# Kernel tuning notes

Hardware: AMD Instinct MI355X
Metric: run time of the kernel (lower is better)

The kernel has to match this reference:

```python
import jax, jax.numpy as jnp
import numpy as np

DIM = 1024
N_HEADS = 16
HEAD_DIM = DIM // N_HEADS
B, S = 1, 4096


def setup_inputs() -> dict:
    key = jax.random.key(0)
    kx, kq, kk, kv, ko = jax.random.split(key, 5)
    scale = 1.0 / np.sqrt(DIM)
    return {
        "x": jax.random.normal(kx, (B, S, DIM), dtype=jnp.float32),
        "Wq": jax.random.normal(kq, (DIM, DIM), dtype=jnp.float32) * scale,
        "Wk": jax.random.normal(kk, (DIM, DIM), dtype=jnp.float32) * scale,
        "Wv": jax.random.normal(kv, (DIM, DIM), dtype=jnp.float32) * scale,
        "Wo": jax.random.normal(ko, (DIM, DIM), dtype=jnp.float32) * scale,
    }


def reference(x, Wq, Wk, Wv, Wo):
    Bb, Ss, D = x.shape
    H, hd = N_HEADS, HEAD_DIM
    # nn.Linear(dim, dim, bias=False): y = x @ W.T
    q = (x @ Wq.T).reshape(Bb, Ss, H, hd).transpose(0, 2, 1, 3)  # [B,H,S,hd]
    k = (x @ Wk.T).reshape(Bb, Ss, H, hd).transpose(0, 2, 1, 3)
    v = (x @ Wv.T).reshape(Bb, Ss, H, hd).transpose(0, 2, 1, 3)
    scores = jnp.einsum("bhqd,bhkd->bhqk", q, k) / np.sqrt(hd)  # [B,H,S,S]
    causal = jnp.triu(jnp.ones((Ss, Ss), dtype=bool), 1)
    scores = jnp.where(causal, -jnp.inf, scores)
    # max-subtract softmax (stable); jax.nn.softmax does the same subtraction
    attn = jax.nn.softmax(scores, axis=-1)
    z = jnp.einsum("bhqk,bhkd->bhqd", attn, v)  # [B,H,S,hd]
    z = z.transpose(0, 2, 1, 3).reshape(Bb, Ss, D)
    return z @ Wo.T
```

## Files before the change

### kernel.cpp

```cpp
#include <hip/hip_runtime.h>
#include <hip/hip_bf16.h>

#define DIM   1024
#define NHEAD 16
#define HD    64
#define SEQ   4096

typedef __attribute__((ext_vector_type(4))) float  f32x4;
typedef __attribute__((ext_vector_type(8))) __bf16 bf16x8;
typedef __attribute__((ext_vector_type(8))) _Float16 f16x8;
typedef __attribute__((ext_vector_type(4))) short  short4v;
typedef __attribute__((ext_vector_type(4))) unsigned uint4v;

template <int B> struct ICt { static constexpr int v = B; };

static __device__ __forceinline__ short f2bf(float f) {
  unsigned u = __builtin_bit_cast(unsigned, f);
  u += 0x7fffu + ((u >> 16) & 1u);
  return (short)(u >> 16);
}
static __device__ __forceinline__ float bflo(unsigned u) {
  return __builtin_bit_cast(float, u << 16);
}
static __device__ __forceinline__ float bfhi(unsigned u) {
  return __builtin_bit_cast(float, u & 0xFFFF0000u);
}

static __device__ __forceinline__ unsigned pkf16(float a, float b) {
  return __builtin_bit_cast(unsigned, __builtin_amdgcn_cvt_pkrtz(a, b));
}

static __device__ __forceinline__ void gl2lds16(const void* g, void* l) {
  __builtin_amdgcn_global_load_lds(
      (__attribute__((address_space(1))) void*)g,
      (__attribute__((address_space(3))) void*)l, 16, 0, 0);
}

__global__ void cast_kernel(const float* __restrict__ x,
                            const float* __restrict__ Wq,
                            const float* __restrict__ Wk,
                            const float* __restrict__ Wv,
                            const float* __restrict__ Wo,
                            short* __restrict__ xb,
                            short* __restrict__ wb) {
  int b = blockIdx.x;
  const float* src;
  short* dst;
  if (b < 4096) {
    src = x + (size_t)b * 1024;
    dst = xb + (size_t)b * 1024;
  } else {
    int t = b - 4096;
    int w = t >> 10;
    size_t off = (size_t)(t & 1023) * 1024;
    src = (w == 0 ? Wq : w == 1 ? Wk : w == 2 ? Wv : Wo) + off;
    dst = wb + (size_t)w * 1048576 + off;
  }
  int i = threadIdx.x;
  float4 v = ((const float4*)src)[i];
  short4v o;
  o.x = f2bf(v.x); o.y = f2bf(v.y); o.z = f2bf(v.z); o.w = f2bf(v.w);
  ((short4v*)dst)[i] = o;
}

template <int OUT>
static __device__ __forceinline__ void gemm_tile(const short* __restrict__ A,
                                                 const short* __restrict__ B,
                                                 void* __restrict__ Cv,
                                                 int N, int K, int bm, int bn,
                                                 short* As, short* Bs) {
  const int tid  = threadIdx.x;
  const int wave = tid >> 6;
  const int lane = tid & 63;
  const int quad = lane >> 4;
  const int l15  = lane & 15;
  const int wm = (wave >> 1) * 64;
  const int wn = (wave & 1) * 64;
  const int sw = (quad ^ ((l15 >> 1) & 3)) * 8;

  f32x4 acc[4][4];
#pragma unroll
  for (int i = 0; i < 4; ++i)
#pragma unroll
    for (int j = 0; j < 4; ++j) acc[i][j] = (f32x4){0.f, 0.f, 0.f, 0.f};

  for (int k0 = 0; k0 < K; k0 += 32) {
#pragma unroll
    for (int it = 0; it < 2; ++it) {
      int c   = it * 256 + wave * 64 + lane;
      int row = c >> 2;
      int ce  = ((c & 3) ^ ((c >> 3) & 3)) * 8;
      gl2lds16(A + (size_t)(bm + row) * K + k0 + ce,
               As + (size_t)(it * 256 + wave * 64) * 8);
      gl2lds16(B + (size_t)(bn + row) * K + k0 + ce,
               Bs + (size_t)(it * 256 + wave * 64) * 8);
    }
    __syncthreads();

    bf16x8 af[4], bfr[4];
#pragma unroll
    for (int mt = 0; mt < 4; ++mt)
      af[mt] = *(const bf16x8*)&As[(wm + mt * 16 + l15) * 32 + sw];
#pragma unroll
    for (int nt = 0; nt < 4; ++nt)
      bfr[nt] = *(const bf16x8*)&Bs[(wn + nt * 16 + l15) * 32 + sw];
#pragma unroll
    for (int mt = 0; mt < 4; ++mt)
#pragma unroll
      for (int nt = 0; nt < 4; ++nt)
        acc[mt][nt] = __builtin_amdgcn_mfma_f32_16x16x32_bf16(
            af[mt], bfr[nt], acc[mt][nt], 0, 0, 0);
    __syncthreads();
  }

  short* C = (short*)Cv;
#pragma unroll
  for (int mt = 0; mt < 4; ++mt)
#pragma unroll
    for (int nt = 0; nt < 4; ++nt)
#pragma unroll
      for (int r = 0; r < 4; ++r) {
        size_t idx = (size_t)(bm + wm + mt * 16 + quad * 4 + r) * N +
                     bn + wn + nt * 16 + l15;
        if (OUT == 0)
          C[idx] = f2bf(acc[mt][nt][r]);
        else
          C[idx] = (short)(pkf16(acc[mt][nt][r], 0.f) & 0xFFFFu);
      }
}

__global__ __launch_bounds__(256, 2) void proj_kernel(const short* __restrict__ xb,
                                                      const short* __restrict__ wqk,
                                                      const short* __restrict__ wv,
                                                      short* __restrict__ QKb,
                                                      short* __restrict__ Vtb) {
  __shared__ short As[128 * 32];
  __shared__ short Bs[128 * 32];
  int b = blockIdx.x;
  if (b < 512) {
    gemm_tile<0>(xb, wqk, QKb, 2048, 1024, (b >> 4) * 128, (b & 15) * 128, As, Bs);
  } else {
    int t = b - 512;
    gemm_tile<2>(wv, xb, Vtb, 4096, 1024, (t >> 5) * 128, (t & 31) * 128, As, Bs);
  }
}

__global__ __launch_bounds__(512, 4) void flash_attn(const short* __restrict__ QK,
                                                     const short* __restrict__ Vt,
                                                     short* __restrict__ pO0,
                                                     short* __restrict__ pO1,
                                                     short* __restrict__ pO2,
                                                     short* __restrict__ pO3,
                                                     float* __restrict__ lp) {
  const int bb  = blockIdx.x;
  const int z   = bb & 3;
  const int h   = (bb >> 2) & 15;
  const int y   = 15 - (bb >> 6);

  __shared__ short Ks[2 * 4096];
  __shared__ short Vs[2 * 4096];

  const int wave = threadIdx.x >> 6;
  const int lane = threadIdx.x & 63;
  const int quad = lane >> 4;
  const int l15  = lane & 15;
  const int qw   = y * 256 + wave * 32;
  const int jtd  = 4 * y + (wave >> 1);

  const short* Qp = QK + h * HD;
  const short* Kp = QK + 1024 + h * HD;
  const short* Vp = Vt + (size_t)(h * HD) * SEQ;

  bf16x8 qf0[2], qf1[2];
#pragma unroll
  for (int kk = 0; kk < 2; ++kk) {
    qf0[kk] = *(const bf16x8*)&Qp[(size_t)(qw + l15) * 2048 + kk * 32 + quad * 8];
    qf1[kk] = *(const bf16x8*)&Qp[(size_t)(qw + 16 + l15) * 2048 + kk * 32 + quad * 8];
  }

  f32x4 oaccA[4], oaccB[4];
  f32x4 laccA = (f32x4){0.f, 0.f, 0.f, 0.f};
  f32x4 laccB = (f32x4){0.f, 0.f, 0.f, 0.f};
#pragma unroll
  for (int nt = 0; nt < 4; ++nt) {
    oaccA[nt] = (f32x4){0.f, 0.f, 0.f, 0.f};
    oaccB[nt] = (f32x4){0.f, 0.f, 0.f, 0.f};
  }

  const float SC = 0.125f * 1.44269504088896340736f;

  f16x8 ones16;
  { uint4v o1 = {0x3C003C00u, 0x3C003C00u, 0x3C003C00u, 0x3C003C00u};
    ones16 = __builtin_bit_cast(f16x8, o1); }

  const short* kq = Ks + quad * 512 + l15 * 8;
  const short* vq = Vs + quad * 512 + l15 * 8;

  const int ow = wave & 3;
  const int hf = wave >> 2;
  const int g = ((lane >> 5) & 1) * 32 + ((lane >> 4) & 1) * 4 +
                ((lane >> 2) & 3) * 8 + (lane & 3);
  const short* kstage = Kp + (size_t)(z * 64 + g) * 2048 + ow * 16 + hf * 8;
  const short* vstage = Vp + (size_t)lane * SEQ + z * 64 + ow * 16 + hf * 8;
  short* ksl = Ks + ow * 1024 + hf * 512;
  short* vsl = Vs + ow * 1024 + hf * 512;
  const size_t KSUB = (size_t)4 * 64 * 2048;
  const int    VSUB = 4 * 64;

  const int qv0 = qw + l15;
  const int qv1 = qw + 16 + l15;

  auto subtile = [&](int jtc, auto bc) {
    constexpr int base = decltype(bc)::v * 4096;
    if (jtc > jtd) return;

    f32x4 s0[4], s1[4];
#pragma unroll
    for (int mt = 0; mt < 4; ++mt) {
      bf16x8 k0 = *(const bf16x8*)(kq + base + mt * 128);
      bf16x8 k1 = *(const bf16x8*)(kq + base + 2048 + mt * 128);
      s0[mt] = (f32x4){0.f, 0.f, 0.f, 0.f};
      s0[mt] = __builtin_amdgcn_mfma_f32_16x16x32_bf16(k0, qf0[0], s0[mt], 0, 0, 0);
      s0[mt] = __builtin_amdgcn_mfma_f32_16x16x32_bf16(k1, qf0[1], s0[mt], 0, 0, 0);
      s1[mt] = (f32x4){0.f, 0.f, 0.f, 0.f};
      s1[mt] = __builtin_amdgcn_mfma_f32_16x16x32_bf16(k0, qf1[0], s1[mt], 0, 0, 0);
      s1[mt] = __builtin_amdgcn_mfma_f32_16x16x32_bf16(k1, qf1[1], s1[mt], 0, 0, 0);
    }

    unsigned pk0[4][2], pk1[4][2];
    const bool domask = (jtc == jtd);
#pragma unroll
    for (int mt = 0; mt < 4; ++mt) {
      float pr[4], qr[4];
#pragma unroll
      for (int r = 0; r < 4; ++r) {
        pr[r] = fmaf(s0[mt][r], SC, -12.0f);
        qr[r] = fmaf(s1[mt][r], SC, -12.0f);
      }
      if (domask) {
        int kb0 = jtc * 64 + (mt >> 1) * 32 + quad * 8 + (mt & 1) * 4;
#pragma unroll
        for (int r = 0; r < 4; ++r) {
          if (kb0 + r > qv0) pr[r] = -1e30f;
          if (kb0 + r > qv1) qr[r] = -1e30f;
        }
      }
#pragma unroll
      for (int r = 0; r < 4; ++r) {
        pr[r] = __builtin_amdgcn_exp2f(pr[r]);
        qr[r] = __builtin_amdgcn_exp2f(qr[r]);
      }
      pk0[mt][0] = pkf16(pr[0], pr[1]);
      pk0[mt][1] = pkf16(pr[2], pr[3]);
      pk1[mt][0] = pkf16(qr[0], qr[1]);
      pk1[mt][1] = pkf16(qr[2], qr[3]);
    }

#pragma unroll
    for (int kk = 0; kk < 2; ++kk) {
      f16x8 vb[4];
#pragma unroll
      for (int nt = 0; nt < 4; ++nt)
        vb[nt] = *(const f16x8*)(vq + base + kk * 2048 + nt * 128);
      f16x8 pa0, pa1;
      { uint4v t = {pk0[2 * kk][0], pk0[2 * kk][1],
                    pk0[2 * kk + 1][0], pk0[2 * kk + 1][1]};
        pa0 = __builtin_bit_cast(f16x8, t); }
      { uint4v t = {pk1[2 * kk][0], pk1[2 * kk][1],
                    pk1[2 * kk + 1][0], pk1[2 * kk + 1][1]};
        pa1 = __builtin_bit_cast(f16x8, t); }
      laccA = __builtin_amdgcn_mfma_f32_16x16x32_f16(pa0, ones16, laccA, 0, 0, 0);
      laccB = __builtin_amdgcn_mfma_f32_16x16x32_f16(pa1, ones16, laccB, 0, 0, 0);
#pragma unroll
      for (int nt = 0; nt < 4; ++nt) {
        oaccA[nt] = __builtin_amdgcn_mfma_f32_16x16x32_f16(pa0, vb[nt], oaccA[nt], 0, 0, 0);
        oaccB[nt] = __builtin_amdgcn_mfma_f32_16x16x32_f16(pa1, vb[nt], oaccB[nt], 0, 0, 0);
      }
    }
  };

  const int nst = y + 1;

  gl2lds16(kstage, ksl);
  gl2lds16(vstage, vsl);
  kstage += KSUB; vstage += VSUB;

  int i = 0, jt = z;
  for (;;) {
    __syncthreads();
    if (i + 1 < nst) {
      gl2lds16(kstage, ksl + 4096);
      gl2lds16(vstage, vsl + 4096);
      kstage += KSUB; vstage += VSUB;
    }
    subtile(jt, ICt<0>{});
    ++i; jt += 4;
    if (i >= nst) break;

    __syncthreads();
    if (i + 1 < nst) {
      gl2lds16(kstage, ksl);
      gl2lds16(vstage, vsl);
      kstage += KSUB; vstage += VSUB;
    }
    subtile(jt, ICt<1>{});
    ++i; jt += 4;
    if (i >= nst) break;
  }

  short* pO = (z == 0) ? pO0 : (z == 1) ? pO1 : (z == 2) ? pO2 : pO3;
#pragma unroll
  for (int nt = 0; nt < 4; ++nt)
#pragma unroll
    for (int r = 0; r < 4; ++r) {
      pO[(size_t)(qw + quad * 4 + r) * DIM + h * HD + nt * 16 + l15] =
          f2bf(oaccA[nt][r]);
      pO[(size_t)(qw + 16 + quad * 4 + r) * DIM + h * HD + nt * 16 + l15] =
          f2bf(oaccB[nt][r]);
    }
  if (l15 == 0) {
#pragma unroll
    for (int r = 0; r < 4; ++r) {
      lp[(size_t)z * SEQ * NHEAD + (size_t)(qw + quad * 4 + r) * NHEAD + h] =
          laccA[r];
      lp[(size_t)z * SEQ * NHEAD + (size_t)(qw + 16 + quad * 4 + r) * NHEAD + h] =
          laccB[r];
    }
  }
}

__global__ void combine_kernel(const short* __restrict__ pO0,
                               const short* __restrict__ pO1,
                               const short* __restrict__ pO2,
                               const short* __restrict__ pO3,
                               const float* __restrict__ lp,
                               short* __restrict__ Z) {
  size_t e = ((size_t)blockIdx.x * 256 + threadIdx.x) * 8;
  int q  = (int)(e >> 10);
  int hh = (int)((e & 1023) >> 6);
  const size_t LS = (size_t)SEQ * NHEAD;
  size_t li = (size_t)q * NHEAD + hh;
  float l = lp[li] + lp[LS + li] + lp[2 * LS + li] + lp[3 * LS + li];
  uint4v a = *(const uint4v*)(pO0 + e);
  uint4v b = *(const uint4v*)(pO1 + e);
  uint4v c = *(const uint4v*)(pO2 + e);
  uint4v d = *(const uint4v*)(pO3 + e);
  float s[8];
#pragma unroll
  for (int i = 0; i < 4; ++i) {
    s[2 * i]     = bflo(a[i]) + bflo(b[i]) + bflo(c[i]) + bflo(d[i]);
    s[2 * i + 1] = bfhi(a[i]) + bfhi(b[i]) + bfhi(c[i]) + bfhi(d[i]);
  }
  float rinv = 1.0f / l;
  uint4v o;
#pragma unroll
  for (int i = 0; i < 4; ++i) {
    unsigned p0 = (unsigned)(unsigned short)f2bf(s[2 * i] * rinv);
    unsigned p1 = (unsigned)(unsigned short)f2bf(s[2 * i + 1] * rinv);
    o[i] = p0 | (p1 << 16);
  }
  *(uint4v*)(Z + e) = o;
}

__global__ __launch_bounds__(256, 2) void gemm_out(const short* __restrict__ A,
                                                   const short* __restrict__ B,
                                                   float* __restrict__ C) {
  __shared__ short As[64 * 32];
  __shared__ short Bs[128 * 32];
  const int tid  = threadIdx.x;
  const int wave = tid >> 6;
  const int lane = tid & 63;
  const int quad = lane >> 4;
  const int l15  = lane & 15;
  const int bm = (int)(blockIdx.x >> 3) * 64;
  const int bn = (int)(blockIdx.x & 7) * 128;
  const int wn = wave * 32;
  const int sw = (quad ^ ((l15 >> 1) & 3)) * 8;

  f32x4 acc[4][2];
#pragma unroll
  for (int i = 0; i < 4; ++i)
#pragma unroll
    for (int j = 0; j < 2; ++j) acc[i][j] = (f32x4){0.f, 0.f, 0.f, 0.f};

  for (int k0 = 0; k0 < 1024; k0 += 32) {
    {
      int c = tid;
      int row = c >> 2;
      int ce = ((c & 3) ^ ((c >> 3) & 3)) * 8;
      gl2lds16(A + (size_t)(bm + row) * 1024 + k0 + ce,
               As + (size_t)(wave * 64) * 8);
    }
#pragma unroll
    for (int it = 0; it < 2; ++it) {
      int c = it * 256 + tid;
      int row = c >> 2;
      int ce = ((c & 3) ^ ((c >> 3) & 3)) * 8;
      gl2lds16(B + (size_t)(bn + row) * 1024 + k0 + ce,
               Bs + (size_t)(it * 256 + wave * 64) * 8);
    }
    __syncthreads();

    bf16x8 af[4], bfr[2];
#pragma unroll
    for (int mt = 0; mt < 4; ++mt)
      af[mt] = *(const bf16x8*)&As[(mt * 16 + l15) * 32 + sw];
#pragma unroll
    for (int nt = 0; nt < 2; ++nt)
      bfr[nt] = *(const bf16x8*)&Bs[(wn + nt * 16 + l15) * 32 + sw];
#pragma unroll
    for (int mt = 0; mt < 4; ++mt)
#pragma unroll
      for (int nt = 0; nt < 2; ++nt)
        acc[mt][nt] = __builtin_amdgcn_mfma_f32_16x16x32_bf16(
            af[mt], bfr[nt], acc[mt][nt], 0, 0, 0);
    __syncthreads();
  }

#pragma unroll
  for (int mt = 0; mt < 4; ++mt)
#pragma unroll
    for (int nt = 0; nt < 2; ++nt)
#pragma unroll
      for (int r = 0; r < 4; ++r)
        C[(size_t)(bm + mt * 16 + quad * 4 + r) * 1024 + bn + wn + nt * 16 + l15] =
            acc[mt][nt][r];
}

extern "C" void kernel_launch(void* const* d_in, const int* in_sizes, int n_in,
                              void* d_out, int out_size, void* d_ws, size_t ws_size,
                              hipStream_t stream) {
  const float* x  = (const float*)d_in[0];
  const float* Wq = (const float*)d_in[1];
  const float* Wk = (const float*)d_in[2];
  const float* Wv = (const float*)d_in[3];
  const float* Wo = (const float*)d_in[4];
  float* out = (float*)d_out;

  char* ws   = (char*)d_ws;
  short* xb  = (short*)(ws);
  short* wqb = (short*)(ws + (size_t)8 * 1024 * 1024);
  short* wvb = wqb + 2 * 1024 * 1024;
  short* wob = wqb + 3 * 1024 * 1024;
  short* QKb = (short*)(ws + (size_t)16 * 1024 * 1024);
  short* Vtb = (short*)(ws + (size_t)32 * 1024 * 1024);
  float* lpb = (float*)(ws + (size_t)8 * 1024 * 1024);
  short* pO0 = (short*)(ws);
  short* pO1 = (short*)(ws + (size_t)40 * 1024 * 1024);
  short* pO2 = (short*)d_out;
  short* pO3 = (short*)d_out + (size_t)4 * 1024 * 1024;
  short* Zb  = QKb;

  cast_kernel<<<dim3(8192), dim3(256), 0, stream>>>(x, Wq, Wk, Wv, Wo, xb, wqb);

  proj_kernel<<<dim3(768), dim3(256), 0, stream>>>(xb, wqb, wvb, QKb, Vtb);

  flash_attn<<<dim3(1024), dim3(512), 0, stream>>>(QKb, Vtb, pO0, pO1, pO2, pO3, lpb);
  combine_kernel<<<dim3(2048), dim3(256), 0, stream>>>(pO0, pO1, pO2, pO3, lpb, Zb);

  gemm_out<<<dim3(512), dim3(256), 0, stream>>>(Zb, wob, out);
}
```

Baseline: 185.8 us.

## Halve flash-attention KV split from four to two with paired subtile staging

```diff
diff --git a/kernel.cpp b/kernel.cpp
--- a/kernel.cpp
+++ b/kernel.cpp
@@ -149,16 +149,15 @@
                                                      const short* __restrict__ Vt,
                                                      short* __restrict__ pO0,
                                                      short* __restrict__ pO1,
-                                                     short* __restrict__ pO2,
-                                                     short* __restrict__ pO3,
                                                      float* __restrict__ lp) {
   const int bb  = blockIdx.x;
-  const int z   = bb & 3;
-  const int h   = (bb >> 2) & 15;
-  const int y   = 15 - (bb >> 6);
-
-  __shared__ short Ks[2 * 4096];
-  __shared__ short Vs[2 * 4096];
+  const int z   = bb & 1;
+  const int h   = (bb >> 1) & 15;
+  const int t   = bb >> 5;
+  const int y   = (t < 8) ? (15 - t) : (t - 8);
+
+  __shared__ short Ks[4 * 4096];
+  __shared__ short Vs[4 * 4096];
 
   const int wave = threadIdx.x >> 6;
   const int lane = threadIdx.x & 63;
@@ -204,8 +203,10 @@
   const short* vstage = Vp + (size_t)lane * SEQ + z * 64 + ow * 16 + hf * 8;
   short* ksl = Ks + ow * 1024 + hf * 512;
   short* vsl = Vs + ow * 1024 + hf * 512;
-  const size_t KSUB = (size_t)4 * 64 * 2048;
-  const int    VSUB = 4 * 64;
+  const size_t KPAIR = (size_t)2 * 64 * 2048;
+  const size_t KADV  = (size_t)4 * 64 * 2048;
+  const int    VPAIR = 2 * 64;
+  const int    VADV  = 4 * 64;
 
   const int qv0 = qw + l15;
   const int qv1 = qw + 16 + l15;
@@ -263,12 +264,12 @@
       for (int nt = 0; nt < 4; ++nt)
         vb[nt] = *(const f16x8*)(vq + base + kk * 2048 + nt * 128);
       f16x8 pa0, pa1;
-      { uint4v t = {pk0[2 * kk][0], pk0[2 * kk][1],
-                    pk0[2 * kk + 1][0], pk0[2 * kk + 1][1]};
-        pa0 = __builtin_bit_cast(f16x8, t); }
-      { uint4v t = {pk1[2 * kk][0], pk1[2 * kk][1],
-                    pk1[2 * kk + 1][0], pk1[2 * kk + 1][1]};
-        pa1 = __builtin_bit_cast(f16x8, t); }
+      { uint4v t2 = {pk0[2 * kk][0], pk0[2 * kk][1],
+                     pk0[2 * kk + 1][0], pk0[2 * kk + 1][1]};
+        pa0 = __builtin_bit_cast(f16x8, t2); }
+      { uint4v t2 = {pk1[2 * kk][0], pk1[2 * kk][1],
+                     pk1[2 * kk + 1][0], pk1[2 * kk + 1][1]};
+        pa1 = __builtin_bit_cast(f16x8, t2); }
       laccA = __builtin_amdgcn_mfma_f32_16x16x32_f16(pa0, ones16, laccA, 0, 0, 0);
       laccB = __builtin_amdgcn_mfma_f32_16x16x32_f16(pa1, ones16, laccB, 0, 0, 0);
 #pragma unroll
@@ -281,34 +282,42 @@
 
   const int nst = y + 1;
 
-  gl2lds16(kstage, ksl);
-  gl2lds16(vstage, vsl);
-  kstage += KSUB; vstage += VSUB;
+  gl2lds16(kstage,         ksl);
+  gl2lds16(kstage + KPAIR, ksl + 4096);
+  gl2lds16(vstage,         vsl);
+  gl2lds16(vstage + VPAIR, vsl + 4096);
+  kstage += KADV; vstage += VADV;
 
   int i = 0, jt = z;
   for (;;) {
     __syncthreads();
     if (i + 1 < nst) {
-      gl2lds16(kstage, ksl + 4096);
-      gl2lds16(vstage, vsl + 4096);
-      kstage += KSUB; vstage += VSUB;
-    }
-    subtile(jt, ICt<0>{});
+      gl2lds16(kstage,         ksl + 8192);
+      gl2lds16(kstage + KPAIR, ksl + 12288);
+      gl2lds16(vstage,         vsl + 8192);
+      gl2lds16(vstage + VPAIR, vsl + 12288);
+      kstage += KADV; vstage += VADV;
+    }
+    subtile(jt,     ICt<0>{});
+    subtile(jt + 2, ICt<1>{});
     ++i; jt += 4;
     if (i >= nst) break;
 
     __syncthreads();
     if (i + 1 < nst) {
-      gl2lds16(kstage, ksl);
-      gl2lds16(vstage, vsl);
-      kstage += KSUB; vstage += VSUB;
-    }
-    subtile(jt, ICt<1>{});
+      gl2lds16(kstage,         ksl);
+      gl2lds16(kstage + KPAIR, ksl + 4096);
+      gl2lds16(vstage,         vsl);
+      gl2lds16(vstage + VPAIR, vsl + 4096);
+      kstage += KADV; vstage += VADV;
+    }
+    subtile(jt,     ICt<2>{});
+    subtile(jt + 2, ICt<3>{});
     ++i; jt += 4;
     if (i >= nst) break;
   }
 
-  short* pO = (z == 0) ? pO0 : (z == 1) ? pO1 : (z == 2) ? pO2 : pO3;
+  short* pO = z ? pO1 : pO0;
 #pragma unroll
   for (int nt = 0; nt < 4; ++nt)
 #pragma unroll
@@ -331,8 +340,6 @@
 
 __global__ void combine_kernel(const short* __restrict__ pO0,
                                const short* __restrict__ pO1,
-                               const short* __restrict__ pO2,
-                               const short* __restrict__ pO3,
                                const float* __restrict__ lp,
                                short* __restrict__ Z) {
   size_t e = ((size_t)blockIdx.x * 256 + threadIdx.x) * 8;
@@ -340,16 +347,14 @@
   int hh = (int)((e & 1023) >> 6);
   const size_t LS = (size_t)SEQ * NHEAD;
   size_t li = (size_t)q * NHEAD + hh;
-  float l = lp[li] + lp[LS + li] + lp[2 * LS + li] + lp[3 * LS + li];
+  float l = lp[li] + lp[LS + li];
   uint4v a = *(const uint4v*)(pO0 + e);
   uint4v b = *(const uint4v*)(pO1 + e);
-  uint4v c = *(const uint4v*)(pO2 + e);
-  uint4v d = *(const uint4v*)(pO3 + e);
   float s[8];
 #pragma unroll
   for (int i = 0; i < 4; ++i) {
-    s[2 * i]     = bflo(a[i]) + bflo(b[i]) + bflo(c[i]) + bflo(d[i]);
-    s[2 * i + 1] = bfhi(a[i]) + bfhi(b[i]) + bfhi(c[i]) + bfhi(d[i]);
+    s[2 * i]     = bflo(a[i]) + bflo(b[i]);
+    s[2 * i + 1] = bfhi(a[i]) + bfhi(b[i]);
   }
   float rinv = 1.0f / l;
   uint4v o;
@@ -447,16 +452,14 @@
   float* lpb = (float*)(ws + (size_t)8 * 1024 * 1024);
   short* pO0 = (short*)(ws);
   short* pO1 = (short*)(ws + (size_t)40 * 1024 * 1024);
-  short* pO2 = (short*)d_out;
-  short* pO3 = (short*)d_out + (size_t)4 * 1024 * 1024;
   short* Zb  = QKb;
 
   cast_kernel<<<dim3(8192), dim3(256), 0, stream>>>(x, Wq, Wk, Wv, Wo, xb, wqb);
 
   proj_kernel<<<dim3(768), dim3(256), 0, stream>>>(xb, wqb, wvb, QKb, Vtb);
 
-  flash_attn<<<dim3(1024), dim3(512), 0, stream>>>(QKb, Vtb, pO0, pO1, pO2, pO3, lpb);
-  combine_kernel<<<dim3(2048), dim3(256), 0, stream>>>(pO0, pO1, pO2, pO3, lpb, Zb);
+  flash_attn<<<dim3(512), dim3(512), 0, stream>>>(QKb, Vtb, pO0, pO1, lpb);
+  combine_kernel<<<dim3(2048), dim3(256), 0, stream>>>(pO0, pO1, lpb, Zb);
 
   gemm_out<<<dim3(512), dim3(256), 0, stream>>>(Zb, wob, out);
 }
```

Result: no change. 186.1 us (+0.2%).
